# Kernel tuning notes

Hardware: AMD Instinct MI355X
Metric: run time of the kernel (lower is better)

## Reference

```python
import jax, jax.numpy as jnp
import numpy as np

N = 100000
E = 1250000
D = 64
POS_DIM = 3


def _linear_params(key, fan_in, fan_out, bias=True):
    k1, k2 = jax.random.split(key)
    bound = 1.0 / np.sqrt(fan_in)
    W = jax.random.uniform(k1, (fan_in, fan_out), minval=-bound, maxval=bound, dtype=jnp.float32)
    if bias:
        b = jax.random.uniform(k2, (fan_out,), minval=-bound, maxval=bound, dtype=jnp.float32)
        return W, b
    return W


def setup_inputs() -> dict:
    key = jax.random.key(0)
    ks = jax.random.split(key, 10)
    x = jax.random.normal(ks[0], (N, D), dtype=jnp.float32)
    pos = jax.random.normal(ks[1], (N, POS_DIM), dtype=jnp.float32)
    edge_index = jax.random.randint(ks[2], (2, E), 0, N, dtype=jnp.int64)
    W_in, b_in = _linear_params(ks[3], D, D)
    W_lin = _linear_params(ks[4], D, D, bias=False)
    W_src = _linear_params(ks[5], D, D, bias=False)
    W_dst = _linear_params(ks[6], D, D, bias=False)
    W_pos, b_pos = _linear_params(ks[7], POS_DIM, D)
    W_out, b_out = _linear_params(ks[8], D, D)
    return {"x": x, "pos": pos, "edge_index": edge_index,
            "W_in": W_in, "b_in": b_in, "W_lin": W_lin, "W_src": W_src,
            "W_dst": W_dst, "W_pos": W_pos, "b_pos": b_pos,
            "W_out": W_out, "b_out": b_out}


def reference(x, pos, edge_index, W_in, b_in, W_lin, W_src, W_dst, W_pos, b_pos, W_out, b_out):
    n = x.shape[0]
    src, dst = edge_index[0], edge_index[1]  # j, i (PyG source_to_target)
    # lin_in + relu
    h = jax.nn.relu(x @ W_in + b_in)  # [N, D]
    # PointTransformerConv projections
    x_lin = h @ W_lin      # value projection, gathered at src (x_j)
    a_src = h @ W_src      # alpha_j side
    a_dst = h @ W_dst      # alpha_i side
    # per-edge positional MLP on pos_i - pos_j
    delta = (pos[dst] - pos[src]) @ W_pos + b_pos  # [E, D]
    # per-edge attention logits, per channel
    alpha = a_dst[dst] - a_src[src] + delta  # [E, D]
    # segment softmax over destination node groups (PyG softmax, eps=1e-16)
    seg_max = jax.ops.segment_max(alpha, dst, num_segments=n)
    alpha = jnp.exp(alpha - seg_max[dst])
    seg_sum = jax.ops.segment_sum(alpha, dst, num_segments=n)
    alpha = alpha / (seg_sum[dst] + 1e-16)
    # weighted messages, scatter-add aggregate
    msg = alpha * (x_lin[src] + delta)  # [E, D]
    out = jax.ops.segment_sum(msg, dst, num_segments=n)  # [N, D]
    # lin_out + relu
    return jax.nn.relu(out @ W_out + b_out)
```

## Files before the change

### kernel.cpp

```cpp
#include <hip/hip_runtime.h>

#define NN 100000
#define NE 1250000
#define NWIN 782
#define GA 256
#define CHUNK ((NE + GA - 1) / GA)
#define CAP16 16
#define OVFCAP 131072
#define WEDCAP 40

typedef __attribute__((ext_vector_type(4))) float f32x4;
typedef __attribute__((ext_vector_type(8))) short s16x8;

__device__ __forceinline__ short bfb(float f) {
    union { float f; unsigned u; } c; c.f = f;
    unsigned u = c.u + 0x7fffu + ((c.u >> 16) & 1u);
    return (short)(u >> 16);
}
__device__ __forceinline__ void splitbf(float v, short& hi, short& lo) {
    hi = bfb(v);
    union { unsigned u; float f; } c; c.u = ((unsigned)(unsigned short)hi) << 16;
    lo = bfb(v - c.f);
}
__device__ __forceinline__ float lo2f(unsigned u) {
    union { unsigned u; float f; } c; c.u = u << 16; return c.f;
}
__device__ __forceinline__ float hi2f(unsigned u) {
    union { unsigned u; float f; } c; c.u = u & 0xffff0000u; return c.f;
}

__global__ __launch_bounds__(256) void k_prep(
    const float* __restrict__ Wi, const float* __restrict__ Wl,
    const float* __restrict__ Ws, const float* __restrict__ Wo,
    short* __restrict__ P, int* __restrict__ ovf_cnt,
    unsigned* __restrict__ AXb)
{
    const int t = blockIdx.x * 256 + threadIdx.x;
    if (t == 0) *ovf_cnt = 0;
    if (t < 64) AXb[(size_t)NN * 64 + t] = 0u;
    if (t >= 2048) return;
    const int mat = t >> 9, rem = t & 511;
    const int lane = rem & 63, cfg = rem >> 6;
    const int kh = cfg >> 2, nt = cfg & 3;
    const int m = lane & 15, q = lane >> 4;
    const float* W = mat == 0 ? Wi : mat == 1 ? Wl : mat == 2 ? Ws : Wo;
    s16x8 v;
    #pragma unroll
    for (int i = 0; i < 8; ++i)
        v[i] = bfb(W[(kh * 32 + q * 8 + i) * 64 + nt * 16 + m]);
    *(s16x8*)&P[(size_t)t * 8] = v;
}

__global__ __launch_bounds__(256) void k_front(
    const int* __restrict__ ei, unsigned* __restrict__ stage, int* __restrict__ gcnt,
    int2* __restrict__ ovf, int* __restrict__ ovf_cnt,
    const float* __restrict__ x, const short* __restrict__ P,
    const float* __restrict__ b_in,
    const float* __restrict__ pos, const float* __restrict__ W_pos,
    unsigned* __restrict__ AXb)
{
    __shared__ int lcnt[NWIN];
    __shared__ float hT[4][16 * 68];

    if (blockIdx.x < GA) {
        const int g = blockIdx.x;
        for (int i = threadIdx.x; i < NWIN; i += 256) lcnt[i] = 0;
        __syncthreads();
        unsigned* myStage = stage + (size_t)g * NWIN * CAP16;
        const int e0 = g * CHUNK;
        const int e1 = (e0 + CHUNK < NE) ? e0 + CHUNK : NE;
        for (int e = e0 + threadIdx.x; e < e1; e += 256) {
            const int s = ei[e], d = ei[NE + e];
            const int b = d >> 7;
            const int c = atomicAdd(&lcnt[b], 1);
            if (c < CAP16) {
                myStage[b * CAP16 + c] = (unsigned)s | ((unsigned)(d & 127) << 17);
            } else {
                const int o = atomicAdd(ovf_cnt, 1);
                if (o < OVFCAP) ovf[o] = make_int2(s, d);
            }
        }
        __syncthreads();
        for (int i = threadIdx.x; i < NWIN; i += 256)
            gcnt[i * GA + g] = lcnt[i] < CAP16 ? lcnt[i] : CAP16;
        return;
    }

    const int lane = threadIdx.x & 63;
    const int wid  = threadIdx.x >> 6;
    const int m = lane & 15, q = lane >> 4;

    s16x8 Wf[3][2][4];
    #pragma unroll
    for (int mat = 0; mat < 3; ++mat)
        #pragma unroll
        for (int kh = 0; kh < 2; ++kh)
            #pragma unroll
            for (int nt = 0; nt < 4; ++nt)
                Wf[mat][kh][nt] = *(const s16x8*)&P[((size_t)mat * 512 + (kh * 4 + nt) * 64 + lane) * 8];
    float bin[4], wpv0[4], wpv1[4], wpv2[4];
    #pragma unroll
    for (int nt = 0; nt < 4; ++nt) {
        bin[nt]  = b_in[nt * 16 + m];
        wpv0[nt] = W_pos[nt * 16 + m];
        wpv1[nt] = W_pos[64 + nt * 16 + m];
        wpv2[nt] = W_pos[128 + nt * 16 + m];
    }

    const int wave = (blockIdx.x - GA) * 4 + wid, nw = (gridDim.x - GA) * 4;
    for (int chunk = wave; chunk < NN / 16; chunk += nw) {
        const int r0 = chunk * 16;
        const float* xr = x + (size_t)(r0 + m) * 64;
        float xv[16];
        *(float4*)&xv[0]  = *(const float4*)(xr + q * 8);
        *(float4*)&xv[4]  = *(const float4*)(xr + q * 8 + 4);
        *(float4*)&xv[8]  = *(const float4*)(xr + 32 + q * 8);
        *(float4*)&xv[12] = *(const float4*)(xr + 32 + q * 8 + 4);
        s16x8 ahi0, alo0, ahi1, alo1;
        #pragma unroll
        for (int i = 0; i < 8; ++i) {
            short h, l;
            splitbf(xv[i], h, l);     ahi0[i] = h; alo0[i] = l;
            splitbf(xv[8 + i], h, l); ahi1[i] = h; alo1[i] = l;
        }
        #pragma unroll
        for (int nt = 0; nt < 4; ++nt) {
            f32x4 acc = {0.f, 0.f, 0.f, 0.f};
            acc = __builtin_amdgcn_mfma_f32_16x16x32_bf16(alo0, Wf[0][0][nt], acc, 0, 0, 0);
            acc = __builtin_amdgcn_mfma_f32_16x16x32_bf16(alo1, Wf[0][1][nt], acc, 0, 0, 0);
            acc = __builtin_amdgcn_mfma_f32_16x16x32_bf16(ahi0, Wf[0][0][nt], acc, 0, 0, 0);
            acc = __builtin_amdgcn_mfma_f32_16x16x32_bf16(ahi1, Wf[0][1][nt], acc, 0, 0, 0);
            #pragma unroll
            for (int r = 0; r < 4; ++r) {
                float hv = acc[r] + bin[nt];
                hT[wid][(q * 4 + r) * 68 + nt * 16 + m] = hv > 0.f ? hv : 0.f;
            }
        }
        float hv[16];
        *(float4*)&hv[0]  = *(const float4*)&hT[wid][m * 68 + q * 8];
        *(float4*)&hv[4]  = *(const float4*)&hT[wid][m * 68 + q * 8 + 4];
        *(float4*)&hv[8]  = *(const float4*)&hT[wid][m * 68 + 32 + q * 8];
        *(float4*)&hv[12] = *(const float4*)&hT[wid][m * 68 + 32 + q * 8 + 4];
        s16x8 hhi0, hlo0, hhi1, hlo1;
        #pragma unroll
        for (int i = 0; i < 8; ++i) {
            short h, l;
            splitbf(hv[i], h, l);     hhi0[i] = h; hlo0[i] = l;
            splitbf(hv[8 + i], h, l); hhi1[i] = h; hlo1[i] = l;
        }
        float px[4], py[4], pz[4];
        #pragma unroll
        for (int r = 0; r < 4; ++r) {
            const float* pp = pos + (size_t)(r0 + q * 4 + r) * 3;
            px[r] = pp[0]; py[r] = pp[1]; pz[r] = pp[2];
        }
        #pragma unroll
        for (int nt = 0; nt < 4; ++nt) {
            f32x4 aS = {0.f, 0.f, 0.f, 0.f}, aL = {0.f, 0.f, 0.f, 0.f};
            aS = __builtin_amdgcn_mfma_f32_16x16x32_bf16(hlo0, Wf[2][0][nt], aS, 0, 0, 0);
            aS = __builtin_amdgcn_mfma_f32_16x16x32_bf16(hlo1, Wf[2][1][nt], aS, 0, 0, 0);
            aS = __builtin_amdgcn_mfma_f32_16x16x32_bf16(hhi0, Wf[2][0][nt], aS, 0, 0, 0);
            aS = __builtin_amdgcn_mfma_f32_16x16x32_bf16(hhi1, Wf[2][1][nt], aS, 0, 0, 0);
            aL = __builtin_amdgcn_mfma_f32_16x16x32_bf16(hlo0, Wf[1][0][nt], aL, 0, 0, 0);
            aL = __builtin_amdgcn_mfma_f32_16x16x32_bf16(hlo1, Wf[1][1][nt], aL, 0, 0, 0);
            aL = __builtin_amdgcn_mfma_f32_16x16x32_bf16(hhi0, Wf[1][0][nt], aL, 0, 0, 0);
            aL = __builtin_amdgcn_mfma_f32_16x16x32_bf16(hhi1, Wf[1][1][nt], aL, 0, 0, 0);
            #pragma unroll
            for (int r = 0; r < 4; ++r) {
                const float sp = fmaf(px[r], wpv0[nt], fmaf(py[r], wpv1[nt], pz[r] * wpv2[nt]));
                const float ev = __expf(-(aS[r] + sp));
                const float ex = ev * (aL[r] - sp);
                const unsigned p = (unsigned)(unsigned short)bfb(ev)
                                 | ((unsigned)(unsigned short)bfb(ex) << 16);
                AXb[(size_t)(r0 + q * 4 + r) * 64 + nt * 16 + m] = p;
            }
        }
    }
}

__global__ __launch_bounds__(256) void k_passB(
    const unsigned* __restrict__ stage, const int* __restrict__ gcnt,
    const int2* __restrict__ ovf, const int* __restrict__ ovf_cnt,
    int* __restrict__ slots, int* __restrict__ deg)
{
    __shared__ int slotsL[128 * WEDCAP];
    __shared__ int cntL[128];
    const int b = blockIdx.x;
    const int t = threadIdx.x;
    if (t < 128) cntL[t] = 0;
    __syncthreads();
    const int n = min(gcnt[b * GA + t], CAP16);
    const unsigned* cell = stage + (size_t)t * NWIN * CAP16 + b * CAP16;
    uint4 q0 = *(const uint4*)cell;
    uint4 q1 = *(const uint4*)(cell + 4);
    uint4 q2 = *(const uint4*)(cell + 8);
    uint4 q3 = *(const uint4*)(cell + 12);
    const unsigned eb[16] = {q0.x, q0.y, q0.z, q0.w, q1.x, q1.y, q1.z, q1.w,
                             q2.x, q2.y, q2.z, q2.w, q3.x, q3.y, q3.z, q3.w};
    #pragma unroll
    for (int i = 0; i < CAP16; ++i)
        if (i < n) {
            const int d7 = (int)(eb[i] >> 17);
            const int c = atomicAdd(&cntL[d7], 1);
            if (c < WEDCAP) slotsL[d7 * WEDCAP + c] = (int)(eb[i] & 0x1ffff);
        }
    const int no = min(*ovf_cnt, OVFCAP);
    for (int i = t; i < no; i += 256) {
        const int2 sd = ovf[i];
        if ((sd.y >> 7) == b) {
            const int d7 = sd.y & 127;
            const int c = atomicAdd(&cntL[d7], 1);
            if (c < WEDCAP) slotsL[d7 * WEDCAP + c] = sd.x;
        }
    }
    __syncthreads();
    int4* dstq = (int4*)(slots + (size_t)b * 128 * WEDCAP);
    const int4* srcq = (const int4*)slotsL;
    #pragma unroll
    for (int i = 0; i < 5; ++i) dstq[i * 256 + t] = srcq[i * 256 + t];
    if (t < 128) {
        const int d = (b << 7) + t;
        if (d < NN) deg[d] = cntL[t] < WEDCAP ? cntL[t] : WEDCAP;
    }
}

__global__ __launch_bounds__(256) void k_agg_out(
    const int* __restrict__ deg_arr, const int* __restrict__ slots,
    const float* __restrict__ pos,
    const float* __restrict__ W_pos, const float* __restrict__ b_pos,
    const unsigned* __restrict__ AXb, const short* __restrict__ P,
    const float* __restrict__ b_out, float* __restrict__ out)
{
    __shared__ float vT[4][16 * 68];
    const int lane = threadIdx.x & 63;
    const int wid  = threadIdx.x >> 6;
    const int m = lane & 15, q = lane >> 4;
    const int base = __builtin_amdgcn_readfirstlane(blockIdx.x * 64 + wid * 16);
    if (base >= NN) return;

    const float wp0 = W_pos[lane], wp1 = W_pos[64 + lane],
                wp2 = W_pos[128 + lane], bp = b_pos[lane];

    for (int t = 0; t < 16; ++t) {
        const int d = base + t;
        float v = 0.f;
        if (d < NN) {
            const float pd0 = pos[d * 3 + 0], pd1 = pos[d * 3 + 1], pd2 = pos[d * 3 + 2];
            const float dlb = fmaf(pd0, wp0, fmaf(pd1, wp1, fmaf(pd2, wp2, bp)));
            int deg = deg_arr[d]; deg = deg < WEDCAP ? deg : WEDCAP;
            const int* srow = slots + (size_t)d * WEDCAP;
            float Sa = 0.f, Ua = 0.f;
            if (deg > 0) {
                int cs[4], ns[4];
                unsigned cax[4], nax[4];
                {
                    const int4 qd = *(const int4*)srow;
                    cs[0] = qd.x;
                    cs[1] = (1 < deg) ? qd.y : NN;
                    cs[2] = (2 < deg) ? qd.z : NN;
                    cs[3] = (3 < deg) ? qd.w : NN;
                    #pragma unroll
                    for (int k = 0; k < 4; ++k)
                        cax[k] = AXb[(unsigned)(cs[k] * 64 + lane)];
                }
                for (int j = 0; j < deg; j += 8) {
                    if (j + 4 < deg) {
                        const int4 qd = *(const int4*)(srow + j + 4);
                        ns[0] = qd.x;
                        ns[1] = (j + 5 < deg) ? qd.y : NN;
                        ns[2] = (j + 6 < deg) ? qd.z : NN;
                        ns[3] = (j + 7 < deg) ? qd.w : NN;
                        #pragma unroll
                        for (int k = 0; k < 4; ++k)
                            nax[k] = AXb[(unsigned)(ns[k] * 64 + lane)];
                    }
                    #pragma unroll
                    for (int k = 0; k < 4; ++k) {
                        Sa += lo2f(cax[k]);
                        Ua += hi2f(cax[k]);
                    }
                    if (j + 8 < deg) {
                        const int4 qd = *(const int4*)(srow + j + 8);
                        cs[0] = qd.x;
                        cs[1] = (j + 9  < deg) ? qd.y : NN;
                        cs[2] = (j + 10 < deg) ? qd.z : NN;
                        cs[3] = (j + 11 < deg) ? qd.w : NN;
                        #pragma unroll
                        for (int k = 0; k < 4; ++k)
                            cax[k] = AXb[(unsigned)(cs[k] * 64 + lane)];
                    }
                    if (j + 4 < deg) {
                        #pragma unroll
                        for (int k = 0; k < 4; ++k) {
                            Sa += lo2f(nax[k]);
                            Ua += hi2f(nax[k]);
                        }
                    }
                }
                v = Ua / (Sa + 1e-16f) + dlb;
            }
        }
        vT[wid][t * 68 + lane] = v;
    }

    s16x8 Wf[2][4];
    #pragma unroll
    for (int kh = 0; kh < 2; ++kh)
        #pragma unroll
        for (int nt = 0; nt < 4; ++nt)
            Wf[kh][nt] = *(const s16x8*)&P[((size_t)3 * 512 + (kh * 4 + nt) * 64 + lane) * 8];
    float bo[4];
    #pragma unroll
    for (int nt = 0; nt < 4; ++nt) bo[nt] = b_out[nt * 16 + m];

    float vv[16];
    *(float4*)&vv[0]  = *(const float4*)&vT[wid][m * 68 + q * 8];
    *(float4*)&vv[4]  = *(const float4*)&vT[wid][m * 68 + q * 8 + 4];
    *(float4*)&vv[8]  = *(const float4*)&vT[wid][m * 68 + 32 + q * 8];
    *(float4*)&vv[12] = *(const float4*)&vT[wid][m * 68 + 32 + q * 8 + 4];
    s16x8 ahi0, alo0, ahi1, alo1;
    #pragma unroll
    for (int i = 0; i < 8; ++i) {
        short h, l;
        splitbf(vv[i], h, l);     ahi0[i] = h; alo0[i] = l;
        splitbf(vv[8 + i], h, l); ahi1[i] = h; alo1[i] = l;
    }
    #pragma unroll
    for (int nt = 0; nt < 4; ++nt) {
        f32x4 acc = {0.f, 0.f, 0.f, 0.f};
        acc = __builtin_amdgcn_mfma_f32_16x16x32_bf16(alo0, Wf[0][nt], acc, 0, 0, 0);
        acc = __builtin_amdgcn_mfma_f32_16x16x32_bf16(alo1, Wf[1][nt], acc, 0, 0, 0);
        acc = __builtin_amdgcn_mfma_f32_16x16x32_bf16(ahi0, Wf[0][nt], acc, 0, 0, 0);
        acc = __builtin_amdgcn_mfma_f32_16x16x32_bf16(ahi1, Wf[1][nt], acc, 0, 0, 0);
        #pragma unroll
        for (int r = 0; r < 4; ++r) {
            const int row = base + q * 4 + r;
            if (row < NN) {
                float o = acc[r] + bo[nt];
                out[(size_t)row * 64 + nt * 16 + m] = o > 0.f ? o : 0.f;
            }
        }
    }
}

extern "C" void kernel_launch(void* const* d_in, const int* in_sizes, int n_in,
                              void* d_out, int out_size, void* d_ws, size_t ws_size,
                              hipStream_t stream) {
    const float* x     = (const float*)d_in[0];
    const float* pos   = (const float*)d_in[1];
    const int*   ei    = (const int*)d_in[2];
    const float* W_in  = (const float*)d_in[3];
    const float* b_in  = (const float*)d_in[4];
    const float* W_lin = (const float*)d_in[5];
    const float* W_src = (const float*)d_in[6];
    const float* W_pos = (const float*)d_in[8];
    const float* b_pos = (const float*)d_in[9];
    const float* W_out = (const float*)d_in[10];
    const float* b_out = (const float*)d_in[11];

    unsigned* AXb   = (unsigned*)d_ws;
    unsigned* stage = AXb + (size_t)(NN + 1) * 64;
    int*      gcnt  = (int*)(stage + (size_t)GA * NWIN * CAP16);
    int*      slots = gcnt + (size_t)NWIN * GA;
    int*      deg   = slots + (size_t)NWIN * 128 * WEDCAP;
    int2*     ovf   = (int2*)(deg + NN);
    int*      ovfc  = (int*)(ovf + OVFCAP);
    short*    P     = (short*)(ovfc + 64);

    k_prep   <<<8,        256, 0, stream>>>(W_in, W_lin, W_src, W_out, P, ovfc, AXb);
    k_front  <<<GA + 512, 256, 0, stream>>>(ei, stage, gcnt, ovf, ovfc,
                                            x, P, b_in, pos, W_pos, AXb);
    k_passB  <<<NWIN,     256, 0, stream>>>(stage, gcnt, ovf, ovfc, slots, deg);
    k_agg_out<<<(NN + 63) / 64, 256, 0, stream>>>(deg, slots, pos, W_pos, b_pos,
                                                  AXb, P, b_out, (float*)d_out);
}
```

Before: 184.0 us.

## Split k_agg_out 16-node tile across four waves sharing one LDS buffer

Each block now handles 16 destination nodes instead of 64. The four waves each aggregate 4 nodes into a shared LDS tile, then after a barrier each wave runs the MFMA epilogue for one 16-column slice of the output. This gives 4x more blocks and a shorter serial gather loop per wave, aimed at more memory-level parallelism and better load balance on the latency-bound gather. It adds a __syncthreads and drops the bounds checks, which relies on NN being divisible by 16.

New measurement: 187.1 us. Within noise of the previous version (+1.7%).

```diff
diff --git a/kernel.cpp b/kernel.cpp
--- a/kernel.cpp
+++ b/kernel.cpp
@@ -231,93 +231,84 @@
     const unsigned* __restrict__ AXb, const short* __restrict__ P,
     const float* __restrict__ b_out, float* __restrict__ out)
 {
-    __shared__ float vT[4][16 * 68];
+    __shared__ float vT[16 * 68];
     const int lane = threadIdx.x & 63;
     const int wid  = threadIdx.x >> 6;
     const int m = lane & 15, q = lane >> 4;
-    const int base = __builtin_amdgcn_readfirstlane(blockIdx.x * 64 + wid * 16);
-    if (base >= NN) return;
+    const int base = __builtin_amdgcn_readfirstlane(blockIdx.x * 16);
 
     const float wp0 = W_pos[lane], wp1 = W_pos[64 + lane],
                 wp2 = W_pos[128 + lane], bp = b_pos[lane];
 
-    for (int t = 0; t < 16; ++t) {
+    for (int i = 0; i < 4; ++i) {
+        const int t = wid * 4 + i;
         const int d = base + t;
-        float v = 0.f;
-        if (d < NN) {
-            const float pd0 = pos[d * 3 + 0], pd1 = pos[d * 3 + 1], pd2 = pos[d * 3 + 2];
-            const float dlb = fmaf(pd0, wp0, fmaf(pd1, wp1, fmaf(pd2, wp2, bp)));
-            int deg = deg_arr[d]; deg = deg < WEDCAP ? deg : WEDCAP;
-            const int* srow = slots + (size_t)d * WEDCAP;
-            float Sa = 0.f, Ua = 0.f;
-            if (deg > 0) {
-                int cs[4], ns[4];
-                unsigned cax[4], nax[4];
-                {
-                    const int4 qd = *(const int4*)srow;
+        const float pd0 = pos[d * 3 + 0], pd1 = pos[d * 3 + 1], pd2 = pos[d * 3 + 2];
+        const float dlb = fmaf(pd0, wp0, fmaf(pd1, wp1, fmaf(pd2, wp2, bp)));
+        int deg = deg_arr[d]; deg = deg < WEDCAP ? deg : WEDCAP;
+        const int* srow = slots + (size_t)d * WEDCAP;
+        float Sa = 0.f, Ua = 0.f;
+        if (deg > 0) {
+            int cs[4], ns[4];
+            unsigned cax[4], nax[4];
+            {
+                const int4 qd = *(const int4*)srow;
+                cs[0] = qd.x;
+                cs[1] = (1 < deg) ? qd.y : NN;
+                cs[2] = (2 < deg) ? qd.z : NN;
+                cs[3] = (3 < deg) ? qd.w : NN;
+                #pragma unroll
+                for (int k = 0; k < 4; ++k)
+                    cax[k] = AXb[(unsigned)(cs[k] * 64 + lane)];
+            }
+            for (int j = 0; j < deg; j += 8) {
+                if (j + 4 < deg) {
+                    const int4 qd = *(const int4*)(srow + j + 4);
+                    ns[0] = qd.x;
+                    ns[1] = (j + 5 < deg) ? qd.y : NN;
+                    ns[2] = (j + 6 < deg) ? qd.z : NN;
+                    ns[3] = (j + 7 < deg) ? qd.w : NN;
+                    #pragma unroll
+                    for (int k = 0; k < 4; ++k)
+                        nax[k] = AXb[(unsigned)(ns[k] * 64 + lane)];
+                }
+                #pragma unroll
+                for (int k = 0; k < 4; ++k) {
+                    Sa += lo2f(cax[k]);
+                    Ua += hi2f(cax[k]);
+                }
+                if (j + 8 < deg) {
+                    const int4 qd = *(const int4*)(srow + j + 8);
                     cs[0] = qd.x;
-                    cs[1] = (1 < deg) ? qd.y : NN;
-                    cs[2] = (2 < deg) ? qd.z : NN;
-                    cs[3] = (3 < deg) ? qd.w : NN;
+                    cs[1] = (j + 9  < deg) ? qd.y : NN;
+                    cs[2] = (j + 10 < deg) ? qd.z : NN;
+                    cs[3] = (j + 11 < deg) ? qd.w : NN;
                     #pragma unroll
                     for (int k = 0; k < 4; ++k)
                         cax[k] = AXb[(unsigned)(cs[k] * 64 + lane)];
                 }
-                for (int j = 0; j < deg; j += 8) {
-                    if (j + 4 < deg) {
-                        const int4 qd = *(const int4*)(srow + j + 4);
-                        ns[0] = qd.x;
-                        ns[1] = (j + 5 < deg) ? qd.y : NN;
-                        ns[2] = (j + 6 < deg) ? qd.z : NN;
-                        ns[3] = (j + 7 < deg) ? qd.w : NN;
-                        #pragma unroll
-                        for (int k = 0; k < 4; ++k)
-                            nax[k] = AXb[(unsigned)(ns[k] * 64 + lane)];
-                    }
+                if (j + 4 < deg) {
                     #pragma unroll
                     for (int k = 0; k < 4; ++k) {
-                        Sa += lo2f(cax[k]);
-                        Ua += hi2f(cax[k]);
-                    }
-                    if (j + 8 < deg) {
-                        const int4 qd = *(const int4*)(srow + j + 8);
-                        cs[0] = qd.x;
-                        cs[1] = (j + 9  < deg) ? qd.y : NN;
-                        cs[2] = (j + 10 < deg) ? qd.z : NN;
-                        cs[3] = (j + 11 < deg) ? qd.w : NN;
-                        #pragma unroll
-                        for (int k = 0; k < 4; ++k)
-                            cax[k] = AXb[(unsigned)(cs[k] * 64 + lane)];
-                    }
-                    if (j + 4 < deg) {
-                        #pragma unroll
-                        for (int k = 0; k < 4; ++k) {
-                            Sa += lo2f(nax[k]);
-                            Ua += hi2f(nax[k]);
-                        }
+                        Sa += lo2f(nax[k]);
+                        Ua += hi2f(nax[k]);
                     }
                 }
-                v = Ua / (Sa + 1e-16f) + dlb;
-            }
-        }
-        vT[wid][t * 68 + lane] = v;
-    }
-
-    s16x8 Wf[2][4];
-    #pragma unroll
-    for (int kh = 0; kh < 2; ++kh)
-        #pragma unroll
-        for (int nt = 0; nt < 4; ++nt)
-            Wf[kh][nt] = *(const s16x8*)&P[((size_t)3 * 512 + (kh * 4 + nt) * 64 + lane) * 8];
-    float bo[4];
-    #pragma unroll
-    for (int nt = 0; nt < 4; ++nt) bo[nt] = b_out[nt * 16 + m];
+            }
+        }
+        vT[t * 68 + lane] = (deg > 0) ? Ua / (Sa + 1e-16f) + dlb : 0.f;
+    }
+    __syncthreads();
+
+    const s16x8 Wf0 = *(const s16x8*)&P[((size_t)3 * 512 + (0 * 4 + wid) * 64 + lane) * 8];
+    const s16x8 Wf1 = *(const s16x8*)&P[((size_t)3 * 512 + (1 * 4 + wid) * 64 + lane) * 8];
+    const float bo = b_out[wid * 16 + m];
 
     float vv[16];
-    *(float4*)&vv[0]  = *(const float4*)&vT[wid][m * 68 + q * 8];
-    *(float4*)&vv[4]  = *(const float4*)&vT[wid][m * 68 + q * 8 + 4];
-    *(float4*)&vv[8]  = *(const float4*)&vT[wid][m * 68 + 32 + q * 8];
-    *(float4*)&vv[12] = *(const float4*)&vT[wid][m * 68 + 32 + q * 8 + 4];
+    *(float4*)&vv[0]  = *(const float4*)&vT[m * 68 + q * 8];
+    *(float4*)&vv[4]  = *(const float4*)&vT[m * 68 + q * 8 + 4];
+    *(float4*)&vv[8]  = *(const float4*)&vT[m * 68 + 32 + q * 8];
+    *(float4*)&vv[12] = *(const float4*)&vT[m * 68 + 32 + q * 8 + 4];
     s16x8 ahi0, alo0, ahi1, alo1;
     #pragma unroll
     for (int i = 0; i < 8; ++i) {
@@ -325,21 +316,15 @@
         splitbf(vv[i], h, l);     ahi0[i] = h; alo0[i] = l;
         splitbf(vv[8 + i], h, l); ahi1[i] = h; alo1[i] = l;
     }
-    #pragma unroll
-    for (int nt = 0; nt < 4; ++nt) {
-        f32x4 acc = {0.f, 0.f, 0.f, 0.f};
-        acc = __builtin_amdgcn_mfma_f32_16x16x32_bf16(alo0, Wf[0][nt], acc, 0, 0, 0);
-        acc = __builtin_amdgcn_mfma_f32_16x16x32_bf16(alo1, Wf[1][nt], acc, 0, 0, 0);
-        acc = __builtin_amdgcn_mfma_f32_16x16x32_bf16(ahi0, Wf[0][nt], acc, 0, 0, 0);
-        acc = __builtin_amdgcn_mfma_f32_16x16x32_bf16(ahi1, Wf[1][nt], acc, 0, 0, 0);
-        #pragma unroll
-        for (int r = 0; r < 4; ++r) {
-            const int row = base + q * 4 + r;
-            if (row < NN) {
-                float o = acc[r] + bo[nt];
-                out[(size_t)row * 64 + nt * 16 + m] = o > 0.f ? o : 0.f;
-            }
-        }
+    f32x4 acc = {0.f, 0.f, 0.f, 0.f};
+    acc = __builtin_amdgcn_mfma_f32_16x16x32_bf16(alo0, Wf0, acc, 0, 0, 0);
+    acc = __builtin_amdgcn_mfma_f32_16x16x32_bf16(alo1, Wf1, acc, 0, 0, 0);
+    acc = __builtin_amdgcn_mfma_f32_16x16x32_bf16(ahi0, Wf0, acc, 0, 0, 0);
+    acc = __builtin_amdgcn_mfma_f32_16x16x32_bf16(ahi1, Wf1, acc, 0, 0, 0);
+    #pragma unroll
+    for (int r = 0; r < 4; ++r) {
+        const float o = acc[r] + bo;
+        out[(size_t)(base + q * 4 + r) * 64 + wid * 16 + m] = o > 0.f ? o : 0.f;
     }
 }
 
@@ -371,6 +356,6 @@
     k_front  <<<GA + 512, 256, 0, stream>>>(ei, stage, gcnt, ovf, ovfc,
                                             x, P, b_in, pos, W_pos, AXb);
     k_passB  <<<NWIN,     256, 0, stream>>>(stage, gcnt, ovf, ovfc, slots, deg);
-    k_agg_out<<<(NN + 63) / 64, 256, 0, stream>>>(deg, slots, pos, W_pos, b_pos,
-                                                  AXb, P, b_out, (float*)d_out);
-}
+    k_agg_out<<<NN / 16,  256, 0, stream>>>(deg, slots, pos, W_pos, b_pos,
+                                            AXb, P, b_out, (float*)d_out);
+}
```

## Fuse bucket binning with aggregation and output projection in one kernel

Applied to the files above, without the earlier changes.

Merges the per-window slot-binning kernel into the aggregation/output kernel, so each 512-thread block bins the edges for its 128 destination nodes into shared memory and then aggregates straight from LDS. This drops the global slots/deg arrays, their writes and reads, and one kernel launch. In exchange each block is larger and uses more shared memory, which may reduce occupancy. The aggregation now waits behind the binning phase inside the block.

Measured after the change: 185.2 us. Within noise of the previous version (+0.7%).

```diff
diff --git a/kernel.cpp b/kernel.cpp
--- a/kernel.cpp
+++ b/kernel.cpp
@@ -178,34 +178,47 @@
     }
 }
 
-__global__ __launch_bounds__(256) void k_passB(
+__global__ __launch_bounds__(512) void k_bin_agg_out(
     const unsigned* __restrict__ stage, const int* __restrict__ gcnt,
     const int2* __restrict__ ovf, const int* __restrict__ ovf_cnt,
-    int* __restrict__ slots, int* __restrict__ deg)
+    const float* __restrict__ pos,
+    const float* __restrict__ W_pos, const float* __restrict__ b_pos,
+    const unsigned* __restrict__ AXb, const short* __restrict__ P,
+    const float* __restrict__ b_out, float* __restrict__ out)
 {
-    __shared__ int slotsL[128 * WEDCAP];
-    __shared__ int cntL[128];
+    __shared__ int   slotsL[128 * WEDCAP];
+    __shared__ int   cntL[128];
+    __shared__ float vT[128 * 68];
     const int b = blockIdx.x;
     const int t = threadIdx.x;
+    const int lane = t & 63;
+    const int wid  = t >> 6;
+    const int m = lane & 15, q = lane >> 4;
+
+    const float wp0 = W_pos[lane], wp1 = W_pos[64 + lane],
+                wp2 = W_pos[128 + lane], bp = b_pos[lane];
+
     if (t < 128) cntL[t] = 0;
     __syncthreads();
-    const int n = min(gcnt[b * GA + t], CAP16);
-    const unsigned* cell = stage + (size_t)t * NWIN * CAP16 + b * CAP16;
-    uint4 q0 = *(const uint4*)cell;
-    uint4 q1 = *(const uint4*)(cell + 4);
-    uint4 q2 = *(const uint4*)(cell + 8);
-    uint4 q3 = *(const uint4*)(cell + 12);
-    const unsigned eb[16] = {q0.x, q0.y, q0.z, q0.w, q1.x, q1.y, q1.z, q1.w,
-                             q2.x, q2.y, q2.z, q2.w, q3.x, q3.y, q3.z, q3.w};
-    #pragma unroll
-    for (int i = 0; i < CAP16; ++i)
-        if (i < n) {
-            const int d7 = (int)(eb[i] >> 17);
-            const int c = atomicAdd(&cntL[d7], 1);
-            if (c < WEDCAP) slotsL[d7 * WEDCAP + c] = (int)(eb[i] & 0x1ffff);
-        }
+    if (t < GA) {
+        const int n = min(gcnt[b * GA + t], CAP16);
+        const unsigned* cell = stage + (size_t)t * NWIN * CAP16 + b * CAP16;
+        uint4 q0 = *(const uint4*)cell;
+        uint4 q1 = *(const uint4*)(cell + 4);
+        uint4 q2 = *(const uint4*)(cell + 8);
+        uint4 q3 = *(const uint4*)(cell + 12);
+        const unsigned eb[16] = {q0.x, q0.y, q0.z, q0.w, q1.x, q1.y, q1.z, q1.w,
+                                 q2.x, q2.y, q2.z, q2.w, q3.x, q3.y, q3.z, q3.w};
+        #pragma unroll
+        for (int i = 0; i < CAP16; ++i)
+            if (i < n) {
+                const int d7 = (int)(eb[i] >> 17);
+                const int c = atomicAdd(&cntL[d7], 1);
+                if (c < WEDCAP) slotsL[d7 * WEDCAP + c] = (int)(eb[i] & 0x1ffff);
+            }
+    }
     const int no = min(*ovf_cnt, OVFCAP);
-    for (int i = t; i < no; i += 256) {
+    for (int i = t; i < no; i += 512) {
         const int2 sd = ovf[i];
         if ((sd.y >> 7) == b) {
             const int d7 = sd.y & 127;
@@ -214,41 +227,17 @@
         }
     }
     __syncthreads();
-    int4* dstq = (int4*)(slots + (size_t)b * 128 * WEDCAP);
-    const int4* srcq = (const int4*)slotsL;
-    #pragma unroll
-    for (int i = 0; i < 5; ++i) dstq[i * 256 + t] = srcq[i * 256 + t];
-    if (t < 128) {
-        const int d = (b << 7) + t;
-        if (d < NN) deg[d] = cntL[t] < WEDCAP ? cntL[t] : WEDCAP;
-    }
-}
-
-__global__ __launch_bounds__(256) void k_agg_out(
-    const int* __restrict__ deg_arr, const int* __restrict__ slots,
-    const float* __restrict__ pos,
-    const float* __restrict__ W_pos, const float* __restrict__ b_pos,
-    const unsigned* __restrict__ AXb, const short* __restrict__ P,
-    const float* __restrict__ b_out, float* __restrict__ out)
-{
-    __shared__ float vT[4][16 * 68];
-    const int lane = threadIdx.x & 63;
-    const int wid  = threadIdx.x >> 6;
-    const int m = lane & 15, q = lane >> 4;
-    const int base = __builtin_amdgcn_readfirstlane(blockIdx.x * 64 + wid * 16);
-    if (base >= NN) return;
-
-    const float wp0 = W_pos[lane], wp1 = W_pos[64 + lane],
-                wp2 = W_pos[128 + lane], bp = b_pos[lane];
-
-    for (int t = 0; t < 16; ++t) {
-        const int d = base + t;
+
+    for (int i2 = 0; i2 < 16; ++i2) {
+        const int tl = wid * 16 + i2;
+        const int d  = b * 128 + tl;
         float v = 0.f;
         if (d < NN) {
             const float pd0 = pos[d * 3 + 0], pd1 = pos[d * 3 + 1], pd2 = pos[d * 3 + 2];
             const float dlb = fmaf(pd0, wp0, fmaf(pd1, wp1, fmaf(pd2, wp2, bp)));
-            int deg = deg_arr[d]; deg = deg < WEDCAP ? deg : WEDCAP;
-            const int* srow = slots + (size_t)d * WEDCAP;
+            int deg = __builtin_amdgcn_readfirstlane(cntL[tl]);
+            deg = deg < WEDCAP ? deg : WEDCAP;
+            const int* srow = &slotsL[tl * WEDCAP];
             float Sa = 0.f, Ua = 0.f;
             if (deg > 0) {
                 int cs[4], ns[4];
@@ -300,7 +289,7 @@
                 v = Ua / (Sa + 1e-16f) + dlb;
             }
         }
-        vT[wid][t * 68 + lane] = v;
+        vT[tl * 68 + lane] = v;
     }
 
     s16x8 Wf[2][4];
@@ -313,11 +302,12 @@
     #pragma unroll
     for (int nt = 0; nt < 4; ++nt) bo[nt] = b_out[nt * 16 + m];
 
+    const int base2 = b * 128 + wid * 16;
     float vv[16];
-    *(float4*)&vv[0]  = *(const float4*)&vT[wid][m * 68 + q * 8];
-    *(float4*)&vv[4]  = *(const float4*)&vT[wid][m * 68 + q * 8 + 4];
-    *(float4*)&vv[8]  = *(const float4*)&vT[wid][m * 68 + 32 + q * 8];
-    *(float4*)&vv[12] = *(const float4*)&vT[wid][m * 68 + 32 + q * 8 + 4];
+    *(float4*)&vv[0]  = *(const float4*)&vT[(wid * 16 + m) * 68 + q * 8];
+    *(float4*)&vv[4]  = *(const float4*)&vT[(wid * 16 + m) * 68 + q * 8 + 4];
+    *(float4*)&vv[8]  = *(const float4*)&vT[(wid * 16 + m) * 68 + 32 + q * 8];
+    *(float4*)&vv[12] = *(const float4*)&vT[(wid * 16 + m) * 68 + 32 + q * 8 + 4];
     s16x8 ahi0, alo0, ahi1, alo1;
     #pragma unroll
     for (int i = 0; i < 8; ++i) {
@@ -334,9 +324,9 @@
         acc = __builtin_amdgcn_mfma_f32_16x16x32_bf16(ahi1, Wf[1][nt], acc, 0, 0, 0);
         #pragma unroll
         for (int r = 0; r < 4; ++r) {
-            const int row = base + q * 4 + r;
+            const int row = base2 + q * 4 + r;
             if (row < NN) {
-                float o = acc[r] + bo[nt];
+                const float o = acc[r] + bo[nt];
                 out[(size_t)row * 64 + nt * 16 + m] = o > 0.f ? o : 0.f;
             }
         }
@@ -361,16 +351,14 @@
     unsigned* AXb   = (unsigned*)d_ws;
     unsigned* stage = AXb + (size_t)(NN + 1) * 64;
     int*      gcnt  = (int*)(stage + (size_t)GA * NWIN * CAP16);
-    int*      slots = gcnt + (size_t)NWIN * GA;
-    int*      deg   = slots + (size_t)NWIN * 128 * WEDCAP;
-    int2*     ovf   = (int2*)(deg + NN);
+    int2*     ovf   = (int2*)(gcnt + (size_t)NWIN * GA);
     int*      ovfc  = (int*)(ovf + OVFCAP);
     short*    P     = (short*)(ovfc + 64);
 
-    k_prep   <<<8,        256, 0, stream>>>(W_in, W_lin, W_src, W_out, P, ovfc, AXb);
-    k_front  <<<GA + 512, 256, 0, stream>>>(ei, stage, gcnt, ovf, ovfc,
-                                            x, P, b_in, pos, W_pos, AXb);
-    k_passB  <<<NWIN,     256, 0, stream>>>(stage, gcnt, ovf, ovfc, slots, deg);
-    k_agg_out<<<(NN + 63) / 64, 256, 0, stream>>>(deg, slots, pos, W_pos, b_pos,
-                                                  AXb, P, b_out, (float*)d_out);
-}
+    k_prep       <<<8,        256, 0, stream>>>(W_in, W_lin, W_src, W_out, P, ovfc, AXb);
+    k_front      <<<GA + 512, 256, 0, stream>>>(ei, stage, gcnt, ovf, ovfc,
+                                                x, P, b_in, pos, W_pos, AXb);
+    k_bin_agg_out<<<NWIN,     512, 0, stream>>>(stage, gcnt, ovf, ovfc, pos,
+                                                W_pos, b_pos, AXb, P, b_out,
+                                                (float*)d_out);
+}
```

## Split 16-node aggregation tile across two waves, single wave does output MFMA

Applied to the files above, without the earlier changes.

The aggregation kernel now assigns each 16-node tile to a 128-thread block. Each of its two waves gathers 8 destination nodes into shared memory, then after a barrier one wave runs the bf16-split MFMA output projection. Before, one wave handled all 16 nodes serially, so this halves the serial gather chain per wave and launches four times as many blocks to hide gather latency. In exchange it adds a block barrier, leaves one wave idle during the MFMA, and drops the bounds checks on the assumption that NN is divisible by 16.

Result: slower. 197.2 us (+7.2%).

```diff
diff --git a/kernel.cpp b/kernel.cpp
--- a/kernel.cpp
+++ b/kernel.cpp
@@ -224,120 +224,116 @@
     }
 }
 
-__global__ __launch_bounds__(256) void k_agg_out(
+__global__ __launch_bounds__(128) void k_agg_out(
     const int* __restrict__ deg_arr, const int* __restrict__ slots,
     const float* __restrict__ pos,
     const float* __restrict__ W_pos, const float* __restrict__ b_pos,
     const unsigned* __restrict__ AXb, const short* __restrict__ P,
     const float* __restrict__ b_out, float* __restrict__ out)
 {
-    __shared__ float vT[4][16 * 68];
+    __shared__ float vT[16 * 68];
     const int lane = threadIdx.x & 63;
     const int wid  = threadIdx.x >> 6;
     const int m = lane & 15, q = lane >> 4;
-    const int base = __builtin_amdgcn_readfirstlane(blockIdx.x * 64 + wid * 16);
-    if (base >= NN) return;
+    const int base = __builtin_amdgcn_readfirstlane(blockIdx.x * 16);
 
     const float wp0 = W_pos[lane], wp1 = W_pos[64 + lane],
                 wp2 = W_pos[128 + lane], bp = b_pos[lane];
 
-    for (int t = 0; t < 16; ++t) {
-        const int d = base + t;
-        float v = 0.f;
-        if (d < NN) {
-            const float pd0 = pos[d * 3 + 0], pd1 = pos[d * 3 + 1], pd2 = pos[d * 3 + 2];
-            const float dlb = fmaf(pd0, wp0, fmaf(pd1, wp1, fmaf(pd2, wp2, bp)));
-            int deg = deg_arr[d]; deg = deg < WEDCAP ? deg : WEDCAP;
-            const int* srow = slots + (size_t)d * WEDCAP;
-            float Sa = 0.f, Ua = 0.f;
-            if (deg > 0) {
-                int cs[4], ns[4];
-                unsigned cax[4], nax[4];
-                {
-                    const int4 qd = *(const int4*)srow;
+    for (int i2 = 0; i2 < 8; ++i2) {
+        const int tl = wid * 8 + i2;
+        const int d  = base + tl;
+        const float pd0 = pos[d * 3 + 0], pd1 = pos[d * 3 + 1], pd2 = pos[d * 3 + 2];
+        const float dlb = fmaf(pd0, wp0, fmaf(pd1, wp1, fmaf(pd2, wp2, bp)));
+        int deg = deg_arr[d]; deg = deg < WEDCAP ? deg : WEDCAP;
+        const int* srow = slots + (size_t)d * WEDCAP;
+        float Sa = 0.f, Ua = 0.f;
+        if (deg > 0) {
+            int cs[4], ns[4];
+            unsigned cax[4], nax[4];
+            {
+                const int4 qd = *(const int4*)srow;
+                cs[0] = qd.x;
+                cs[1] = (1 < deg) ? qd.y : NN;
+                cs[2] = (2 < deg) ? qd.z : NN;
+                cs[3] = (3 < deg) ? qd.w : NN;
+                #pragma unroll
+                for (int k = 0; k < 4; ++k)
+                    cax[k] = AXb[(unsigned)(cs[k] * 64 + lane)];
+            }
+            for (int j = 0; j < deg; j += 8) {
+                if (j + 4 < deg) {
+                    const int4 qd = *(const int4*)(srow + j + 4);
+                    ns[0] = qd.x;
+                    ns[1] = (j + 5 < deg) ? qd.y : NN;
+                    ns[2] = (j + 6 < deg) ? qd.z : NN;
+                    ns[3] = (j + 7 < deg) ? qd.w : NN;
+                    #pragma unroll
+                    for (int k = 0; k < 4; ++k)
+                        nax[k] = AXb[(unsigned)(ns[k] * 64 + lane)];
+                }
+                #pragma unroll
+                for (int k = 0; k < 4; ++k) {
+                    Sa += lo2f(cax[k]);
+                    Ua += hi2f(cax[k]);
+                }
+                if (j + 8 < deg) {
+                    const int4 qd = *(const int4*)(srow + j + 8);
                     cs[0] = qd.x;
-                    cs[1] = (1 < deg) ? qd.y : NN;
-                    cs[2] = (2 < deg) ? qd.z : NN;
-                    cs[3] = (3 < deg) ? qd.w : NN;
+                    cs[1] = (j + 9  < deg) ? qd.y : NN;
+                    cs[2] = (j + 10 < deg) ? qd.z : NN;
+                    cs[3] = (j + 11 < deg) ? qd.w : NN;
                     #pragma unroll
                     for (int k = 0; k < 4; ++k)
                         cax[k] = AXb[(unsigned)(cs[k] * 64 + lane)];
                 }
-                for (int j = 0; j < deg; j += 8) {
-                    if (j + 4 < deg) {
-                        const int4 qd = *(const int4*)(srow + j + 4);
-                        ns[0] = qd.x;
-                        ns[1] = (j + 5 < deg) ? qd.y : NN;
-                        ns[2] = (j + 6 < deg) ? qd.z : NN;
-                        ns[3] = (j + 7 < deg) ? qd.w : NN;
-                        #pragma unroll
-                        for (int k = 0; k < 4; ++k)
-                            nax[k] = AXb[(unsigned)(ns[k] * 64 + lane)];
-                    }
+                if (j + 4 < deg) {
                     #pragma unroll
                     for (int k = 0; k < 4; ++k) {
-                        Sa += lo2f(cax[k]);
-                        Ua += hi2f(cax[k]);
-                    }
-                    if (j + 8 < deg) {
-                        const int4 qd = *(const int4*)(srow + j + 8);
-                        cs[0] = qd.x;
-                        cs[1] = (j + 9  < deg) ? qd.y : NN;
-                        cs[2] = (j + 10 < deg) ? qd.z : NN;
-                        cs[3] = (j + 11 < deg) ? qd.w : NN;
-                        #pragma unroll
-                        for (int k = 0; k < 4; ++k)
-                            cax[k] = AXb[(unsigned)(cs[k] * 64 + lane)];
-                    }
-                    if (j + 4 < deg) {
-                        #pragma unroll
-                        for (int k = 0; k < 4; ++k) {
-                            Sa += lo2f(nax[k]);
-                            Ua += hi2f(nax[k]);
-                        }
+                        Sa += lo2f(nax[k]);
+                        Ua += hi2f(nax[k]);
                     }
                 }
-                v = Ua / (Sa + 1e-16f) + dlb;
-            }
-        }
-        vT[wid][t * 68 + lane] = v;
-    }
-
-    s16x8 Wf[2][4];
-    #pragma unroll
-    for (int kh = 0; kh < 2; ++kh)
-        #pragma unroll
-        for (int nt = 0; nt < 4; ++nt)
-            Wf[kh][nt] = *(const s16x8*)&P[((size_t)3 * 512 + (kh * 4 + nt) * 64 + lane) * 8];
-    float bo[4];
-    #pragma unroll
-    for (int nt = 0; nt < 4; ++nt) bo[nt] = b_out[nt * 16 + m];
-
-    float vv[16];
-    *(float4*)&vv[0]  = *(const float4*)&vT[wid][m * 68 + q * 8];
-    *(float4*)&vv[4]  = *(const float4*)&vT[wid][m * 68 + q * 8 + 4];
-    *(float4*)&vv[8]  = *(const float4*)&vT[wid][m * 68 + 32 + q * 8];
-    *(float4*)&vv[12] = *(const float4*)&vT[wid][m * 68 + 32 + q * 8 + 4];
-    s16x8 ahi0, alo0, ahi1, alo1;
-    #pragma unroll
-    for (int i = 0; i < 8; ++i) {
-        short h, l;
-        splitbf(vv[i], h, l);     ahi0[i] = h; alo0[i] = l;
-        splitbf(vv[8 + i], h, l); ahi1[i] = h; alo1[i] = l;
-    }
-    #pragma unroll
-    for (int nt = 0; nt < 4; ++nt) {
-        f32x4 acc = {0.f, 0.f, 0.f, 0.f};
-        acc = __builtin_amdgcn_mfma_f32_16x16x32_bf16(alo0, Wf[0][nt], acc, 0, 0, 0);
-        acc = __builtin_amdgcn_mfma_f32_16x16x32_bf16(alo1, Wf[1][nt], acc, 0, 0, 0);
-        acc = __builtin_amdgcn_mfma_f32_16x16x32_bf16(ahi0, Wf[0][nt], acc, 0, 0, 0);
-        acc = __builtin_amdgcn_mfma_f32_16x16x32_bf16(ahi1, Wf[1][nt], acc, 0, 0, 0);
-        #pragma unroll
-        for (int r = 0; r < 4; ++r) {
-            const int row = base + q * 4 + r;
-            if (row < NN) {
-                float o = acc[r] + bo[nt];
-                out[(size_t)row * 64 + nt * 16 + m] = o > 0.f ? o : 0.f;
+            }
+        }
+        vT[tl * 68 + lane] = (deg > 0) ? Ua / (Sa + 1e-16f) + dlb : 0.f;
+    }
+    __syncthreads();
+
+    if (wid == 0) {
+        s16x8 Wf[2][4];
+        #pragma unroll
+        for (int kh = 0; kh < 2; ++kh)
+            #pragma unroll
+            for (int nt = 0; nt < 4; ++nt)
+                Wf[kh][nt] = *(const s16x8*)&P[((size_t)3 * 512 + (kh * 4 + nt) * 64 + lane) * 8];
+        float bo[4];
+        #pragma unroll
+        for (int nt = 0; nt < 4; ++nt) bo[nt] = b_out[nt * 16 + m];
+
+        float vv[16];
+        *(float4*)&vv[0]  = *(const float4*)&vT[m * 68 + q * 8];
+        *(float4*)&vv[4]  = *(const float4*)&vT[m * 68 + q * 8 + 4];
+        *(float4*)&vv[8]  = *(const float4*)&vT[m * 68 + 32 + q * 8];
+        *(float4*)&vv[12] = *(const float4*)&vT[m * 68 + 32 + q * 8 + 4];
+        s16x8 ahi0, alo0, ahi1, alo1;
+        #pragma unroll
+        for (int i = 0; i < 8; ++i) {
+            short h, l;
+            splitbf(vv[i], h, l);     ahi0[i] = h; alo0[i] = l;
+            splitbf(vv[8 + i], h, l); ahi1[i] = h; alo1[i] = l;
+        }
+        #pragma unroll
+        for (int nt = 0; nt < 4; ++nt) {
+            f32x4 acc = {0.f, 0.f, 0.f, 0.f};
+            acc = __builtin_amdgcn_mfma_f32_16x16x32_bf16(alo0, Wf[0][nt], acc, 0, 0, 0);
+            acc = __builtin_amdgcn_mfma_f32_16x16x32_bf16(alo1, Wf[1][nt], acc, 0, 0, 0);
+            acc = __builtin_amdgcn_mfma_f32_16x16x32_bf16(ahi0, Wf[0][nt], acc, 0, 0, 0);
+            acc = __builtin_amdgcn_mfma_f32_16x16x32_bf16(ahi1, Wf[1][nt], acc, 0, 0, 0);
+            #pragma unroll
+            for (int r = 0; r < 4; ++r) {
+                const float o = acc[r] + bo[nt];
+                out[(size_t)(base + q * 4 + r) * 64 + nt * 16 + m] = o > 0.f ? o : 0.f;
             }
         }
     }
@@ -371,6 +367,6 @@
     k_front  <<<GA + 512, 256, 0, stream>>>(ei, stage, gcnt, ovf, ovfc,
                                             x, P, b_in, pos, W_pos, AXb);
     k_passB  <<<NWIN,     256, 0, stream>>>(stage, gcnt, ovf, ovfc, slots, deg);
-    k_agg_out<<<(NN + 63) / 64, 256, 0, stream>>>(deg, slots, pos, W_pos, b_pos,
-                                                  AXb, P, b_out, (float*)d_out);
-}
+    k_agg_out<<<NN / 16,  128, 0, stream>>>(deg, slots, pos, W_pos, b_pos,
+                                            AXb, P, b_out, (float*)d_out);
+}
```
